# Kernel optimization log

Measured on AMD Instinct MI355X. Metric: run time of the kernel, lower is better.

The kernel has to match this reference:

```python
import jax, jax.numpy as jnp
import numpy as np

SL, BS, HS, FFN = 2048, 1, 512, 2048
E, TOP_K = 8, 2


def setup_inputs() -> dict:
    key = jax.random.key(0)
    k_x, k_w, k_i, k_w1, k_w2 = jax.random.split(key, 5)
    x = jax.random.normal(k_x, (SL, BS, HS), dtype=jnp.float32)
    expert_weights = jax.random.uniform(k_w, (SL * BS, TOP_K), dtype=jnp.float32)
    expert_indices = jax.random.randint(k_i, (SL * BS, TOP_K), 0, E, dtype=jnp.int32)
    # grouped expert MLP params (megablocks GroupedMLP, regular type, no bias)
    w1 = jax.random.normal(k_w1, (E, HS, FFN), dtype=jnp.float32) * (HS ** -0.5)
    w2 = jax.random.normal(k_w2, (E, FFN, HS), dtype=jnp.float32) * (FFN ** -0.5)
    return {"x": x, "expert_weights": expert_weights, "expert_indices": expert_indices,
            "w1": w1, "w2": w2}


def reference(x, expert_weights, expert_indices, w1, w2):
    sl, bs, hs = x.shape
    n_tok = sl * bs
    xf = x.reshape(n_tok, hs)                      # [N, hs]
    ew = expert_weights.reshape(-1)                # [N*top_k]
    ei = expert_indices.reshape(-1)                # [N*top_k]

    # indices_and_bins: stable radix sort of assignments by expert id
    indices = jnp.argsort(ei)                      # stable in jax -> sorted assignment ids
    bin_ids = ei[indices]                          # sorted expert id per assignment

    # megablocks gather: row for assignment i is indices[i] // top_k
    rows = indices // TOP_K                        # [T]
    xg = xf[rows]                                  # [T, hs] expert-contiguous tokens

    # grouped GEMM expert MLP (dense masked loop over fixed expert count)
    outg = jnp.zeros_like(xg)
    for e in range(E):
        m = (bin_ids == e).astype(x.dtype)[:, None]
        h = jax.nn.gelu(xg @ w1[e], approximate=False)   # [T, ffn]
        outg = outg + m * (h @ w2[e])                    # [T, hs]

    # buffer.index_add_(0, E*input_indices + bin_ids, output.detach())
    buf_idx = E * rows + bin_ids
    buffer = jnp.zeros((n_tok * E, hs), x.dtype).at[buf_idx].add(
        jax.lax.stop_gradient(outg))

    # megablocks scatter: weighted combine back to token order
    y = jnp.zeros((n_tok, hs), x.dtype).at[rows].add(outg * ew[indices][:, None])
    return y.reshape(sl, bs, hs), buffer.reshape(n_tok, E, hs)
```

## Files before the change

kernel.cpp:

```cpp
#include <hip/hip_runtime.h>
#include <hip/hip_bf16.h>

#define NTOK 2048
#define TOPK 2
#define HS   512
#define FFN  2048
#define NE   8
#define TASSIGN (NTOK*TOPK)
#define PAD  5120
#define MAXT128 40
#define MAXT64  72

typedef __attribute__((ext_vector_type(8))) short bf16x8;
typedef __attribute__((ext_vector_type(4))) float f32x4;

static const size_t OFF_XBF  = 0;
static const size_t OFF_W1T  = 2097152;
static const size_t OFF_W2T  = 18874368;
static const size_t OFF_H    = 35651584;
static const size_t OFF_OUTV = 56623104;
static const size_t OFF_RT   = 77594624;
static const size_t OFF_HROF = 77615104;
static const size_t OFF_TE128= 77631488;
static const size_t OFF_TR128= 77631648;
static const size_t OFF_TE64 = 77631808;
static const size_t OFF_TR64 = 77632096;

__device__ __forceinline__ unsigned short f2bf(float f) {
    union { __hip_bfloat16 h; unsigned short u; } v;
    v.h = __float2bfloat16(f);
    return v.u;
}

__device__ __forceinline__ int swz(int r, int byte_off) {
    return byte_off ^ ((r & 7) << 4);
}

#define GLOAD16(gsrc, ldst) \
    __builtin_amdgcn_global_load_lds((const __attribute__((address_space(1))) void*)(gsrc), \
                                     (__attribute__((address_space(3))) void*)(ldst), 16, 0, 0)

__device__ __forceinline__ void tr_strip(const float* __restrict__ in,
                                         unsigned short* __restrict__ out,
                                         int R, int C, int e, int rb, int cb0, int ncb,
                                         int tid, unsigned short* t) {
    int tx = tid & 31, ty = tid >> 5;
    const float* ip = in + (size_t)e * R * C;
    unsigned short* op = out + (size_t)e * C * R;
#pragma unroll 1
    for (int it = 0; it < ncb; ++it) {
        int cb = (cb0 + it) * 32;
        __syncthreads();
#pragma unroll
        for (int i = 0; i < 4; i++) {
            int r = ty + i * 8;
            t[r * 33 + tx] = f2bf(ip[(size_t)(rb + r) * C + cb + tx]);
        }
        __syncthreads();
#pragma unroll
        for (int i = 0; i < 4; i++) {
            int c = ty + i * 8;
            op[(size_t)(cb + c) * R + rb + tx] = t[tx * 33 + c];
        }
    }
}

__global__ __launch_bounds__(256) void k_prep1(
        const float* __restrict__ x, const float* __restrict__ w1,
        const int* __restrict__ ei,
        unsigned short* __restrict__ xbf, unsigned short* __restrict__ w1T,
        int* __restrict__ rowtok, int* __restrict__ hrof,
        int* __restrict__ te128, int* __restrict__ tr128,
        int* __restrict__ te64, int* __restrict__ tr64) {
    __shared__ unsigned short tsh[32 * 33];
    int b = blockIdx.x;
    int tid = threadIdx.x;
    if (b == 0) {
        __shared__ int cnt[NE], offpad[NE], cur[NE];
        for (int i = tid; i < PAD; i += 256) rowtok[i] = 0;
        if (tid < NE) cnt[tid] = 0;
        __syncthreads();
        for (int a = tid; a < TASSIGN; a += 256) atomicAdd(&cnt[ei[a]], 1);
        __syncthreads();
        if (tid == 0) {
            int o = 0, t1 = 0, t2 = 0;
            for (int e = 0; e < NE; e++) {
                offpad[e] = o; cur[e] = 0;
                for (int r = 0; r < cnt[e]; r += 128) { te128[t1] = e; tr128[t1] = o + r; t1++; }
                for (int r = 0; r < cnt[e]; r += 64)  { te64[t2]  = e; tr64[t2]  = o + r; t2++; }
                o += (cnt[e] + 127) / 128 * 128;
            }
            for (; t1 < MAXT128; t1++) te128[t1] = -1;
            for (; t2 < MAXT64;  t2++) te64[t2]  = -1;
        }
        __syncthreads();
        for (int a = tid; a < TASSIGN; a += 256) {
            int e = ei[a];
            int r = atomicAdd(&cur[e], 1);
            int hr = offpad[e] + r;
            rowtok[hr] = a >> 1;
            hrof[a] = hr;
        }
    } else if (b < 1 + 1024) {
        int i = ((b - 1) * 256 + tid) * 4;
        float4 v = *(const float4*)(x + i);
        ushort4 o;
        o.x = f2bf(v.x); o.y = f2bf(v.y); o.z = f2bf(v.z); o.w = f2bf(v.w);
        *(ushort4*)(xbf + i) = o;
    } else {
        int blk = b - 1025;
        int e = blk >> 6, rem = blk & 63;
        int rbt = rem >> 2, q = rem & 3;
        tr_strip(w1, w1T, HS, FFN, e, rbt * 32, q * 16, 16, tid, tsh);
    }
}

__global__ __launch_bounds__(256) void k_g1w2t(
        const unsigned short* __restrict__ A,
        const unsigned short* __restrict__ B,
        unsigned short* __restrict__ Hout,
        const int* __restrict__ rowtok,
        const int* __restrict__ te, const int* __restrict__ tr,
        const float* __restrict__ w2, unsigned short* __restrict__ w2T) {
    __shared__ int4 smem4[49152 / 16];
    int b = blockIdx.x;
    int tid = threadIdx.x;

    if (b >= 1280) {
        int blk = b - 1280;
        int e = blk >> 6, rbt = blk & 63;
        tr_strip(w2, w2T, FFN, HS, e, rbt * 32, 0, 16, tid, (unsigned short*)smem4);
        return;
    }

    constexpr int BM = 128, BN = 64, K = HS;
    constexpr int MI = 4, NJ = 2, PA = 4, PB = 2;
    constexpr int ABYTES = BM * 64 * 2, BBYTES = BN * 64 * 2;
    constexpr int NSTEP = K / 64;
    constexpr int N = FFN;

    int ct = b & 31;
    int mt = b >> 5;
    int e = te[mt];
    if (e < 0) return;
    int hr0 = tr[mt];

    char* A0 = (char*)smem4;
    char* A1 = A0 + ABYTES;
    char* B0 = A1 + ABYTES;
    char* B1 = B0 + BBYTES;

    int lane = tid & 63, wave = tid >> 6;
    int wm = wave >> 1, wn = wave & 1;

    const char* asrc[PA];
    const char* bsrc[PB];
    int adoff[PA], bdoff[PB];
#pragma unroll
    for (int p = 0; p < PA; p++) {
        int idx = p * 256 + tid;
        int r = idx >> 3, c8 = idx & 7;
        int c8s = c8 ^ (r & 7);
        size_t row = (size_t)rowtok[hr0 + r];
        asrc[p] = (const char*)(A + row * K) + c8s * 16;
        adoff[p] = (p * 256 + wave * 64) * 16;
    }
#pragma unroll
    for (int p = 0; p < PB; p++) {
        int idx = p * 256 + tid;
        int r = idx >> 3, c8 = idx & 7;
        int c8s = c8 ^ (r & 7);
        bsrc[p] = (const char*)(B + ((size_t)e * N + (size_t)ct * BN + r) * K) + c8s * 16;
        bdoff[p] = (p * 256 + wave * 64) * 16;
    }

    f32x4 acc[MI][NJ] = {};

    auto stage = [&](char* Ad, char* Bd, int s) {
        int kb = s * 128;
#pragma unroll
        for (int p = 0; p < PA; p++) GLOAD16(asrc[p] + kb, Ad + adoff[p]);
#pragma unroll
        for (int p = 0; p < PB; p++) GLOAD16(bsrc[p] + kb, Bd + bdoff[p]);
    };
    auto compute = [&](const char* As, const char* Bs) {
#pragma unroll
        for (int kk = 0; kk < 64; kk += 32) {
            bf16x8 af[MI], bfv[NJ];
#pragma unroll
            for (int i = 0; i < MI; i++) {
                int ar = wm * (BM / 2) + i * 16 + (lane & 15);
                af[i] = *(const bf16x8*)(As + swz(ar, ar * 128 + kk * 2 + (lane >> 4) * 16));
            }
#pragma unroll
            for (int j = 0; j < NJ; j++) {
                int bc = wn * (BN / 2) + j * 16 + (lane & 15);
                bfv[j] = *(const bf16x8*)(Bs + swz(bc, bc * 128 + kk * 2 + (lane >> 4) * 16));
            }
#pragma unroll
            for (int i = 0; i < MI; i++)
#pragma unroll
                for (int j = 0; j < NJ; j++)
                    acc[i][j] = __builtin_amdgcn_mfma_f32_16x16x32_bf16(af[i], bfv[j], acc[i][j], 0, 0, 0);
        }
    };

    stage(A0, B0, 0);
    __syncthreads();
#pragma unroll 1
    for (int s = 0; s < NSTEP; s += 2) {
        if (s + 1 < NSTEP) stage(A1, B1, s + 1);
        compute(A0, B0);
        __syncthreads();
        if (s + 2 < NSTEP) stage(A0, B0, s + 2);
        compute(A1, B1);
        __syncthreads();
    }

#pragma unroll
    for (int i = 0; i < MI; i++)
#pragma unroll
        for (int j = 0; j < NJ; j++)
#pragma unroll
            for (int q = 0; q < 4; q++) {
                int row = hr0 + wm * (BM / 2) + i * 16 + (lane >> 4) * 4 + q;
                int col = ct * BN + wn * (BN / 2) + j * 16 + (lane & 15);
                float v = acc[i][j][q];
                float g = 0.5f * v * (1.0f + erff(v * 0.70710678118f));
                Hout[(size_t)row * N + col] = f2bf(g);
            }
}

template<int BM, int BN, int KFULL, int KLOC>
__global__ __launch_bounds__(256) void k_gemm2(
        const unsigned short* __restrict__ A,
        const unsigned short* __restrict__ B,
        float* __restrict__ outp,
        const int* __restrict__ te, const int* __restrict__ tr, int N) {
    constexpr int MI = BM / 32, NJ = BN / 32;
    constexpr int PA = BM / 32, PB = BN / 32;
    constexpr int ABYTES = BM * 64 * 2, BBYTES = BN * 64 * 2;
    constexpr int NSTEP = KLOC / 64;
    static_assert(NSTEP % 2 == 0, "even steps");

    int mt = blockIdx.y;
    int e = te[mt];
    if (e < 0) return;
    int hr0 = tr[mt];
    int ct = blockIdx.x;
    int kz = blockIdx.z;
    int k0 = kz * KLOC;

    __shared__ int4 ldsv[(2 * (ABYTES + BBYTES)) / 16];
    char* A0 = (char*)ldsv;
    char* A1 = A0 + ABYTES;
    char* B0 = A1 + ABYTES;
    char* B1 = B0 + BBYTES;

    int tid = threadIdx.x;
    int lane = tid & 63, wave = tid >> 6;
    int wm = wave >> 1, wn = wave & 1;

    const char* asrc[PA];
    const char* bsrc[PB];
    int adoff[PA], bdoff[PB];
#pragma unroll
    for (int p = 0; p < PA; p++) {
        int idx = p * 256 + tid;
        int r = idx >> 3, c8 = idx & 7;
        int c8s = c8 ^ (r & 7);
        asrc[p] = (const char*)(A + (size_t)(hr0 + r) * KFULL + k0) + c8s * 16;
        adoff[p] = (p * 256 + wave * 64) * 16;
    }
#pragma unroll
    for (int p = 0; p < PB; p++) {
        int idx = p * 256 + tid;
        int r = idx >> 3, c8 = idx & 7;
        int c8s = c8 ^ (r & 7);
        bsrc[p] = (const char*)(B + ((size_t)e * N + (size_t)ct * BN + r) * KFULL + k0) + c8s * 16;
        bdoff[p] = (p * 256 + wave * 64) * 16;
    }

    f32x4 acc[MI][NJ] = {};

    auto stage = [&](char* Ad, char* Bd, int s) {
        int kb = s * 128;
#pragma unroll
        for (int p = 0; p < PA; p++) GLOAD16(asrc[p] + kb, Ad + adoff[p]);
#pragma unroll
        for (int p = 0; p < PB; p++) GLOAD16(bsrc[p] + kb, Bd + bdoff[p]);
    };
    auto compute = [&](const char* As, const char* Bs) {
#pragma unroll
        for (int kk = 0; kk < 64; kk += 32) {
            bf16x8 af[MI], bfv[NJ];
#pragma unroll
            for (int i = 0; i < MI; i++) {
                int ar = wm * (BM / 2) + i * 16 + (lane & 15);
                af[i] = *(const bf16x8*)(As + swz(ar, ar * 128 + kk * 2 + (lane >> 4) * 16));
            }
#pragma unroll
            for (int j = 0; j < NJ; j++) {
                int bc = wn * (BN / 2) + j * 16 + (lane & 15);
                bfv[j] = *(const bf16x8*)(Bs + swz(bc, bc * 128 + kk * 2 + (lane >> 4) * 16));
            }
#pragma unroll
            for (int i = 0; i < MI; i++)
#pragma unroll
                for (int j = 0; j < NJ; j++)
                    acc[i][j] = __builtin_amdgcn_mfma_f32_16x16x32_bf16(af[i], bfv[j], acc[i][j], 0, 0, 0);
        }
    };

    stage(A0, B0, 0);
    __syncthreads();
#pragma unroll 1
    for (int s = 0; s < NSTEP; s += 2) {
        if (s + 1 < NSTEP) stage(A1, B1, s + 1);
        compute(A0, B0);
        __syncthreads();
        if (s + 2 < NSTEP) stage(A0, B0, s + 2);
        compute(A1, B1);
        __syncthreads();
    }

    float* O = outp + (size_t)kz * PAD * HS;
#pragma unroll
    for (int i = 0; i < MI; i++)
#pragma unroll
        for (int j = 0; j < NJ; j++)
#pragma unroll
            for (int q = 0; q < 4; q++) {
                int row = hr0 + wm * (BM / 2) + i * 16 + (lane >> 4) * 4 + q;
                int col = ct * BN + wn * (BN / 2) + j * 16 + (lane & 15);
                O[(size_t)row * N + col] = acc[i][j][q];
            }
}

__global__ __launch_bounds__(256) void k_combine(
        const float4* __restrict__ outv, const int* __restrict__ ei,
        const float* __restrict__ ew, const int* __restrict__ hrof,
        float4* __restrict__ y, float4* __restrict__ buf) {
    constexpr int SPLIT_OFF = PAD * HS / 4;
    int g = blockIdx.x * 256 + threadIdx.x;
    int t = g >> 7, c4 = g & 127;
    int a0 = 2 * t, a1 = a0 + 1;
    int h0 = hrof[a0], h1 = hrof[a1];
    float4 p0a = outv[(size_t)h0 * (HS / 4) + c4];
    float4 p0b = outv[SPLIT_OFF + (size_t)h0 * (HS / 4) + c4];
    float4 p1a = outv[(size_t)h1 * (HS / 4) + c4];
    float4 p1b = outv[SPLIT_OFF + (size_t)h1 * (HS / 4) + c4];
    float4 o0 = make_float4(p0a.x + p0b.x, p0a.y + p0b.y, p0a.z + p0b.z, p0a.w + p0b.w);
    float4 o1 = make_float4(p1a.x + p1b.x, p1a.y + p1b.y, p1a.z + p1b.z, p1a.w + p1b.w);
    float w0 = ew[a0], w1 = ew[a1];
    y[g] = make_float4(w0 * o0.x + w1 * o1.x, w0 * o0.y + w1 * o1.y,
                       w0 * o0.z + w1 * o1.z, w0 * o0.w + w1 * o1.w);
    int e0 = ei[a0], e1 = ei[a1];
    size_t base = (size_t)t * (NE * HS / 4) + c4;
#pragma unroll
    for (int e = 0; e < NE; e++) {
        float4 v = make_float4(0.f, 0.f, 0.f, 0.f);
        if (e == e0) { v.x += o0.x; v.y += o0.y; v.z += o0.z; v.w += o0.w; }
        if (e == e1) { v.x += o1.x; v.y += o1.y; v.z += o1.z; v.w += o1.w; }
        buf[base + (size_t)e * (HS / 4)] = v;
    }
}

extern "C" void kernel_launch(void* const* d_in, const int* in_sizes, int n_in,
                              void* d_out, int out_size, void* d_ws, size_t ws_size,
                              hipStream_t stream) {
    const float* x  = (const float*)d_in[0];
    const float* ew = (const float*)d_in[1];
    const int*   ei = (const int*)d_in[2];
    const float* w1 = (const float*)d_in[3];
    const float* w2 = (const float*)d_in[4];

    char* ws = (char*)d_ws;
    unsigned short* xbf  = (unsigned short*)(ws + OFF_XBF);
    unsigned short* w1T  = (unsigned short*)(ws + OFF_W1T);
    unsigned short* w2T  = (unsigned short*)(ws + OFF_W2T);
    unsigned short* Hb   = (unsigned short*)(ws + OFF_H);
    float*          outv = (float*)(ws + OFF_OUTV);
    int*            rowtok = (int*)(ws + OFF_RT);
    int*            hrof   = (int*)(ws + OFF_HROF);
    int*            te128  = (int*)(ws + OFF_TE128);
    int*            tr128  = (int*)(ws + OFF_TR128);
    int*            te64   = (int*)(ws + OFF_TE64);
    int*            tr64   = (int*)(ws + OFF_TR64);

    float* y   = (float*)d_out;
    float* buf = (float*)d_out + (size_t)NTOK * HS;

    k_prep1<<<1537, 256, 0, stream>>>(
        x, w1, ei, xbf, w1T, rowtok, hrof, te128, tr128, te64, tr64);
    k_g1w2t<<<1792, 256, 0, stream>>>(
        xbf, w1T, Hb, rowtok, te128, tr128, w2, w2T);
    k_gemm2<64, 64, FFN, FFN / 2><<<dim3(HS / 64, MAXT64, 2), 256, 0, stream>>>(
        Hb, w2T, outv, te64, tr64, HS);
    k_combine<<<NTOK * HS / 4 / 256, 256, 0, stream>>>(
        (const float4*)outv, ei, ew, hrof, (float4*)y, (float4*)buf);
}
```

Before: 95.00 us.

## Store split-K GEMM2 partials in bf16 and run w2 transpose blocks first

The second grouped GEMM now writes its split-K partial outputs as bf16 instead of fp32, which halves the intermediate buffer's write and read traffic. The combine kernel reads eight bf16 values per thread and widens them to fp32. Separately, the w2-transpose blocks in the fused GEMM1 kernel move to the front of the grid so they are scheduled first rather than as a tail. Rounding the partials to bf16 adds precision loss before the fp32 sum and weighted combine.

```diff
diff --git a/kernel.cpp b/kernel.cpp
--- a/kernel.cpp
+++ b/kernel.cpp
@@ -12,6 +12,7 @@
 #define MAXT64  72
 
 typedef __attribute__((ext_vector_type(8))) short bf16x8;
+typedef __attribute__((ext_vector_type(8))) unsigned short u16x8;
 typedef __attribute__((ext_vector_type(4))) float f32x4;
 
 static const size_t OFF_XBF  = 0;
@@ -19,17 +20,23 @@
 static const size_t OFF_W2T  = 18874368;
 static const size_t OFF_H    = 35651584;
 static const size_t OFF_OUTV = 56623104;
-static const size_t OFF_RT   = 77594624;
-static const size_t OFF_HROF = 77615104;
-static const size_t OFF_TE128= 77631488;
-static const size_t OFF_TR128= 77631648;
-static const size_t OFF_TE64 = 77631808;
-static const size_t OFF_TR64 = 77632096;
+static const size_t OFF_RT   = 67108864;
+static const size_t OFF_HROF = 67129344;
+static const size_t OFF_TE128= 67145728;
+static const size_t OFF_TR128= 67145888;
+static const size_t OFF_TE64 = 67146048;
+static const size_t OFF_TR64 = 67146336;
 
 __device__ __forceinline__ unsigned short f2bf(float f) {
     union { __hip_bfloat16 h; unsigned short u; } v;
     v.h = __float2bfloat16(f);
     return v.u;
+}
+
+__device__ __forceinline__ float bf2f(unsigned short u) {
+    union { unsigned int i; float f; } v;
+    v.i = ((unsigned int)u) << 16;
+    return v.f;
 }
 
 __device__ __forceinline__ int swz(int r, int byte_off) {
@@ -126,9 +133,8 @@
     int b = blockIdx.x;
     int tid = threadIdx.x;
 
-    if (b >= 1280) {
-        int blk = b - 1280;
-        int e = blk >> 6, rbt = blk & 63;
+    if (b < 512) {
+        int e = b >> 6, rbt = b & 63;
         tr_strip(w2, w2T, FFN, HS, e, rbt * 32, 0, 16, tid, (unsigned short*)smem4);
         return;
     }
@@ -139,8 +145,9 @@
     constexpr int NSTEP = K / 64;
     constexpr int N = FFN;
 
-    int ct = b & 31;
-    int mt = b >> 5;
+    int bb = b - 512;
+    int ct = bb & 31;
+    int mt = bb >> 5;
     int e = te[mt];
     if (e < 0) return;
     int hr0 = tr[mt];
@@ -235,7 +242,7 @@
 __global__ __launch_bounds__(256) void k_gemm2(
         const unsigned short* __restrict__ A,
         const unsigned short* __restrict__ B,
-        float* __restrict__ outp,
+        unsigned short* __restrict__ outp,
         const int* __restrict__ te, const int* __restrict__ tr, int N) {
     constexpr int MI = BM / 32, NJ = BN / 32;
     constexpr int PA = BM / 32, PB = BN / 32;
@@ -324,7 +331,7 @@
         __syncthreads();
     }
 
-    float* O = outp + (size_t)kz * PAD * HS;
+    unsigned short* O = outp + (size_t)kz * PAD * HS;
 #pragma unroll
     for (int i = 0; i < MI; i++)
 #pragma unroll
@@ -333,36 +340,45 @@
             for (int q = 0; q < 4; q++) {
                 int row = hr0 + wm * (BM / 2) + i * 16 + (lane >> 4) * 4 + q;
                 int col = ct * BN + wn * (BN / 2) + j * 16 + (lane & 15);
-                O[(size_t)row * N + col] = acc[i][j][q];
+                O[(size_t)row * N + col] = f2bf(acc[i][j][q]);
             }
 }
 
 __global__ __launch_bounds__(256) void k_combine(
-        const float4* __restrict__ outv, const int* __restrict__ ei,
+        const unsigned short* __restrict__ outv, const int* __restrict__ ei,
         const float* __restrict__ ew, const int* __restrict__ hrof,
-        float4* __restrict__ y, float4* __restrict__ buf) {
-    constexpr int SPLIT_OFF = PAD * HS / 4;
+        float* __restrict__ y, float* __restrict__ buf) {
+    constexpr size_t SPLIT = (size_t)PAD * HS;
     int g = blockIdx.x * 256 + threadIdx.x;
-    int t = g >> 7, c4 = g & 127;
+    int t = g >> 6, c8 = g & 63;
     int a0 = 2 * t, a1 = a0 + 1;
     int h0 = hrof[a0], h1 = hrof[a1];
-    float4 p0a = outv[(size_t)h0 * (HS / 4) + c4];
-    float4 p0b = outv[SPLIT_OFF + (size_t)h0 * (HS / 4) + c4];
-    float4 p1a = outv[(size_t)h1 * (HS / 4) + c4];
-    float4 p1b = outv[SPLIT_OFF + (size_t)h1 * (HS / 4) + c4];
-    float4 o0 = make_float4(p0a.x + p0b.x, p0a.y + p0b.y, p0a.z + p0b.z, p0a.w + p0b.w);
-    float4 o1 = make_float4(p1a.x + p1b.x, p1a.y + p1b.y, p1a.z + p1b.z, p1a.w + p1b.w);
+    u16x8 q0a = *(const u16x8*)(outv + (size_t)h0 * HS + c8 * 8);
+    u16x8 q0b = *(const u16x8*)(outv + SPLIT + (size_t)h0 * HS + c8 * 8);
+    u16x8 q1a = *(const u16x8*)(outv + (size_t)h1 * HS + c8 * 8);
+    u16x8 q1b = *(const u16x8*)(outv + SPLIT + (size_t)h1 * HS + c8 * 8);
     float w0 = ew[a0], w1 = ew[a1];
-    y[g] = make_float4(w0 * o0.x + w1 * o1.x, w0 * o0.y + w1 * o1.y,
-                       w0 * o0.z + w1 * o1.z, w0 * o0.w + w1 * o1.w);
+    float o0[8], o1[8], yy[8];
+#pragma unroll
+    for (int k = 0; k < 8; k++) {
+        o0[k] = bf2f(q0a[k]) + bf2f(q0b[k]);
+        o1[k] = bf2f(q1a[k]) + bf2f(q1b[k]);
+        yy[k] = w0 * o0[k] + w1 * o1[k];
+    }
+    float* yp = y + (size_t)t * HS + c8 * 8;
+    *(float4*)(yp)     = make_float4(yy[0], yy[1], yy[2], yy[3]);
+    *(float4*)(yp + 4) = make_float4(yy[4], yy[5], yy[6], yy[7]);
     int e0 = ei[a0], e1 = ei[a1];
-    size_t base = (size_t)t * (NE * HS / 4) + c4;
+    float* bt = buf + (size_t)t * (NE * HS) + c8 * 8;
 #pragma unroll
     for (int e = 0; e < NE; e++) {
-        float4 v = make_float4(0.f, 0.f, 0.f, 0.f);
-        if (e == e0) { v.x += o0.x; v.y += o0.y; v.z += o0.z; v.w += o0.w; }
-        if (e == e1) { v.x += o1.x; v.y += o1.y; v.z += o1.z; v.w += o1.w; }
-        buf[base + (size_t)e * (HS / 4)] = v;
+        float v[8];
+#pragma unroll
+        for (int k = 0; k < 8; k++)
+            v[k] = (e == e0 ? o0[k] : 0.0f) + (e == e1 ? o1[k] : 0.0f);
+        float* be = bt + (size_t)e * HS;
+        *(float4*)(be)     = make_float4(v[0], v[1], v[2], v[3]);
+        *(float4*)(be + 4) = make_float4(v[4], v[5], v[6], v[7]);
     }
 }
 
@@ -380,7 +396,7 @@
     unsigned short* w1T  = (unsigned short*)(ws + OFF_W1T);
     unsigned short* w2T  = (unsigned short*)(ws + OFF_W2T);
     unsigned short* Hb   = (unsigned short*)(ws + OFF_H);
-    float*          outv = (float*)(ws + OFF_OUTV);
+    unsigned short* outv = (unsigned short*)(ws + OFF_OUTV);
     int*            rowtok = (int*)(ws + OFF_RT);
     int*            hrof   = (int*)(ws + OFF_HROF);
     int*            te128  = (int*)(ws + OFF_TE128);
@@ -397,6 +413,6 @@
         xbf, w1T, Hb, rowtok, te128, tr128, w2, w2T);
     k_gemm2<64, 64, FFN, FFN / 2><<<dim3(HS / 64, MAXT64, 2), 256, 0, stream>>>(
         Hb, w2T, outv, te64, tr64, HS);
-    k_combine<<<NTOK * HS / 4 / 256, 256, 0, stream>>>(
-        (const float4*)outv, ei, ew, hrof, (float4*)y, (float4*)buf);
-}
+    k_combine<<<NTOK * HS / 8 / 256, 256, 0, stream>>>(
+        outv, ei, ew, hrof, y, buf);
+}
```

Result: no change. 94.16 us (-0.9%).
